# Performance work log

Measured on AMD Instinct MI355X. Metric: run time of the kernel, lower is better.

Reference implementation:

```python
import jax, jax.numpy as jnp
import numpy as np

B, N, M, D_MODEL, D_K, D_V = 8, 2048, 2048, 1024, 1024, 1024
NEG = -1000000000.0


def setup_inputs() -> dict:
    key = jax.random.key(0)
    ks = jax.random.split(key, 10)
    s = 1.0 / np.sqrt(D_MODEL)
    return {
        "querys": jax.random.normal(ks[0], (B, N, D_MODEL), jnp.float32),
        "keys": jax.random.normal(ks[1], (B, M, D_MODEL), jnp.float32),
        "values": jax.random.normal(ks[2], (B, M, D_MODEL), jnp.float32),
        "mask": jax.random.randint(ks[3], (N, M), 0, 2, jnp.int32),
        "Wq": jax.random.normal(ks[4], (D_K, D_MODEL), jnp.float32) * s,
        "bq": jnp.zeros((D_K,), jnp.float32),
        "Wk": jax.random.normal(ks[5], (D_K, D_MODEL), jnp.float32) * s,
        "bk": jnp.zeros((D_K,), jnp.float32),
        "Wv": jax.random.normal(ks[6], (D_V, D_MODEL), jnp.float32) * s,
        "bv": jnp.zeros((D_V,), jnp.float32),
    }


def reference(querys, keys, values, mask, Wq, bq, Wk, bk, Wv, bv):
    # Linear projections (torch Linear: x @ W.T + b)
    q = querys @ Wq.T + bq          # [B, N, Dk]
    k = keys @ Wk.T + bk            # [B, M, Dk]
    v = values @ Wv.T + bv          # [B, M, Dv]
    # Original computes QK^T via broadcast mul+sum; GEMM form is identical math.
    # NOTE: no 1/sqrt(d) scaling, matching the source.
    scores = jnp.einsum('bnd,bmd->bnm', q, k)  # [B, N, M]
    scores = jnp.where(mask[None, :, :] == 0, NEG, scores)
    weights = jax.nn.softmax(scores, axis=2)
    out = jnp.einsum('bnm,bmd->bnd', weights, v)  # [B, N, Dv]
    return out
```

## Files before the change

### kernel.cpp

```cpp
#include <hip/hip_runtime.h>
#include <cstdint>

typedef __bf16 bf16_t;
typedef __bf16 bf16x8 __attribute__((ext_vector_type(8)));
typedef float f32x4 __attribute__((ext_vector_type(4)));

#define AS1 __attribute__((address_space(1)))
#define AS3 __attribute__((address_space(3)))

__device__ __forceinline__ void gload_lds16(const bf16_t* g, bf16_t* l) {
    __builtin_amdgcn_global_load_lds((const AS1 void*)g, (AS3 void*)l, 16, 0, 0);
}
__device__ __forceinline__ f32x4 mfma_bf16(bf16x8 a, bf16x8 b, f32x4 c) {
    return __builtin_amdgcn_mfma_f32_16x16x32_bf16(a, b, c, 0, 0, 0);
}

template <bool SPLIT, int BIAS, int OUTMODE>
__global__ __launch_bounds__(512, 2) void gemm256(
    const bf16_t* __restrict__ Ah, const bf16_t* __restrict__ Al, long long strideA, int lda,
    const bf16_t* __restrict__ Bh, const bf16_t* __restrict__ Bl, long long strideB, int ldb,
    void* __restrict__ C0, void* __restrict__ C1, long long strideC, int ldc,
    const float* __restrict__ bias, int K)
{
    __shared__ bf16_t lds[4 * 16384];

    int bx = blockIdx.x, by = blockIdx.y, bz = blockIdx.z;
    {
        const int gx = gridDim.x, gy = gridDim.y, gz = gridDim.z;
        const int n = gx * gy * gz;
        if ((n & 7) == 0) {
            int lin = bx + gx * (by + gy * bz);
            lin = (lin & 7) * (n >> 3) + (lin >> 3);
            bx = lin % gx; lin /= gx;
            by = lin % gy; bz = lin / gy;
        }
    }

    const int rowBase = by * 256;
    const int colBase = bx * 256;
    const bf16_t* AhB = Ah + (long long)bz * strideA;
    const bf16_t* BhB = Bh + (long long)bz * strideB;
    const bf16_t* AlB = SPLIT ? Al + (long long)bz * strideA : nullptr;
    const bf16_t* BlB = SPLIT ? Bl + (long long)bz * strideB : nullptr;

    const int t = threadIdx.x;
    const int lane = t & 63;
    const int w = t >> 6;
    const int wm = w >> 2;
    const int wn = w & 3;

    const int r0 = t >> 2;
    const int sl8 = ((t & 3) ^ ((r0 >> 1) & 3)) * 8;
    const long long aoff0 = (long long)(rowBase + r0) * lda + sl8;
    const long long aoff1 = (long long)(rowBase + r0 + 128) * lda + sl8;
    const long long boff0 = (long long)(colBase + r0) * ldb + sl8;
    const long long boff1 = (long long)(colBase + r0 + 128) * ldb + sl8;

    const int NT = SPLIT ? (K >> 5) * 3 : (K >> 5);

    auto tsrc = [&](int jt, const bf16_t*& sA, const bf16_t*& sB, long long& k0) {
        if (SPLIT) {
            const int chunk = jt / 3;
            const int term = jt - chunk * 3;
            k0 = (long long)chunk * 32;
            sA = (term == 2) ? AlB : AhB;
            sB = (term == 1) ? BlB : BhB;
        } else {
            k0 = (long long)jt * 32;
            sA = AhB; sB = BhB;
        }
    };

    f32x4 acc[8][4] = {};

    for (int jt = 0; jt < 3; ++jt) {
        const bf16_t *sA, *sB; long long k0;
        tsrc(jt, sA, sB, k0);
        bf16_t* db = lds + jt * 16384;
        gload_lds16(sA + aoff0 + k0, db + t * 8);
        gload_lds16(sA + aoff1 + k0, db + 4096 + t * 8);
        gload_lds16(sB + boff0 + k0, db + 8192 + t * 8);
        gload_lds16(sB + boff1 + k0, db + 12288 + t * 8);
    }
    asm volatile("s_waitcnt vmcnt(8)" ::: "memory");
    __builtin_amdgcn_s_barrier();

    const int fr = lane & 15;
    const int kqs = ((lane >> 4) ^ ((lane >> 1) & 3)) * 8;

    for (int j = 0; j < NT; ++j) {
        const bf16_t* bufA = lds + (j & 3) * 16384;
        const bf16_t* bufB = bufA + 8192;

        const int jt = j + 3;
        if (jt < NT) {
            const bf16_t *sA, *sB; long long k0;
            tsrc(jt, sA, sB, k0);
            bf16_t* db = lds + (jt & 3) * 16384;
            gload_lds16(sA + aoff0 + k0, db + t * 8);
            gload_lds16(sA + aoff1 + k0, db + 4096 + t * 8);
            gload_lds16(sB + boff0 + k0, db + 8192 + t * 8);
            gload_lds16(sB + boff1 + k0, db + 12288 + t * 8);
        }

        bf16x8 a[8], b[4];
#pragma unroll
        for (int mi = 0; mi < 8; mi++)
            a[mi] = *(const bf16x8*)&bufA[(wm * 128 + mi * 16 + fr) * 32 + kqs];
#pragma unroll
        for (int ni = 0; ni < 4; ni++)
            b[ni] = *(const bf16x8*)&bufB[(wn * 64 + ni * 16 + fr) * 32 + kqs];

        __builtin_amdgcn_s_setprio(1);
#pragma unroll
        for (int mi = 0; mi < 8; mi++)
#pragma unroll
            for (int ni = 0; ni < 4; ni++)
                acc[mi][ni] = mfma_bf16(a[mi], b[ni], acc[mi][ni]);
        __builtin_amdgcn_s_setprio(0);

        if (j + 1 < NT) {
            if (j < NT - 3)       asm volatile("s_waitcnt vmcnt(8)" ::: "memory");
            else if (j == NT - 3) asm volatile("s_waitcnt vmcnt(4)" ::: "memory");
            else                  asm volatile("s_waitcnt vmcnt(0)" ::: "memory");
            __builtin_amdgcn_s_barrier();
        }
    }

    const int fc = lane & 15;
    const int fr4 = (lane >> 4) * 4;
#pragma unroll
    for (int mi = 0; mi < 8; mi++)
#pragma unroll
        for (int ni = 0; ni < 4; ni++)
#pragma unroll
            for (int rg = 0; rg < 4; rg++) {
                const int row = rowBase + wm * 128 + mi * 16 + fr4 + rg;
                const int col = colBase + wn * 64 + ni * 16 + fc;
                float v = acc[mi][ni][rg];
                if (BIAS == 1) v += bias[col];
                else if (BIAS == 2) v += bias[row];
                const long long off = (long long)bz * strideC + (long long)row * ldc + col;
                if (OUTMODE == 0) {
                    ((float*)C0)[off] = v;
                } else if (OUTMODE == 1) {
                    ((bf16_t*)C0)[off] = (bf16_t)v;
                } else {
                    const bf16_t h = (bf16_t)v;
                    ((bf16_t*)C0)[off] = h;
                    ((bf16_t*)C1)[off] = (bf16_t)(v - (float)h);
                }
            }
}

__global__ __launch_bounds__(256) void split_f32(const float* __restrict__ x,
                                                 bf16_t* __restrict__ h,
                                                 bf16_t* __restrict__ l)
{
    const long long i = ((long long)blockIdx.x * 256 + threadIdx.x) * 4;
    const float4 v = *(const float4*)&x[i];
    bf16_t hh[4], ll[4];
    const float vv[4] = {v.x, v.y, v.z, v.w};
#pragma unroll
    for (int j = 0; j < 4; j++) {
        hh[j] = (bf16_t)vv[j];
        ll[j] = (bf16_t)(vv[j] - (float)hh[j]);
    }
    *(short4*)&h[i] = *(short4*)hh;
    *(short4*)&l[i] = *(short4*)ll;
}

__global__ __launch_bounds__(256) void cast_f32(const float* __restrict__ x,
                                                bf16_t* __restrict__ y)
{
    const long long i = ((long long)blockIdx.x * 256 + threadIdx.x) * 4;
    const float4 v = *(const float4*)&x[i];
    bf16_t hh[4] = {(bf16_t)v.x, (bf16_t)v.y, (bf16_t)v.z, (bf16_t)v.w};
    *(short4*)&y[i] = *(short4*)hh;
}

__global__ __launch_bounds__(256) void softmax_rows(const float* __restrict__ S,
                                                    bf16_t* __restrict__ P,
                                                    const int* __restrict__ mask,
                                                    int n0)
{
    __shared__ float red[4];
    const long long r = blockIdx.x;
    const float* row = S + r * 2048;
    const int* mrow = mask + (long long)(n0 + (int)(r & 2047)) * 2048;
    const int t = threadIdx.x;

    float v[8];
#pragma unroll
    for (int i = 0; i < 8; i++) {
        const int j = i * 256 + t;
        v[i] = (mrow[j] != 0) ? row[j] : -1000000000.0f;
    }
    float m = v[0];
#pragma unroll
    for (int i = 1; i < 8; i++) m = fmaxf(m, v[i]);
#pragma unroll
    for (int off = 32; off; off >>= 1) m = fmaxf(m, __shfl_xor(m, off));
    if ((t & 63) == 0) red[t >> 6] = m;
    __syncthreads();
    const float rowmax = fmaxf(fmaxf(red[0], red[1]), fmaxf(red[2], red[3]));
    __syncthreads();

    float sum = 0.0f;
    float e[8];
#pragma unroll
    for (int i = 0; i < 8; i++) { e[i] = __expf(v[i] - rowmax); sum += e[i]; }
#pragma unroll
    for (int off = 32; off; off >>= 1) sum += __shfl_xor(sum, off);
    if ((t & 63) == 0) red[t >> 6] = sum;
    __syncthreads();
    const float inv = 1.0f / (red[0] + red[1] + red[2] + red[3]);

    bf16_t* prow = P + r * 2048;
#pragma unroll
    for (int i = 0; i < 8; i++) prow[i * 256 + t] = (bf16_t)(e[i] * inv);
}

extern "C" void kernel_launch(void* const* d_in, const int* in_sizes, int n_in,
                              void* d_out, int out_size, void* d_ws, size_t ws_size,
                              hipStream_t stream) {
    constexpr int Bb = 8, N = 2048, M = 2048, D = 1024;
    constexpr long long MB = 1LL << 20;

    const float* querys = (const float*)d_in[0];
    const float* keys   = (const float*)d_in[1];
    const float* values = (const float*)d_in[2];
    const int*   mask   = (const int*)d_in[3];
    const float* Wq = (const float*)d_in[4];
    const float* bq = (const float*)d_in[5];
    const float* Wk = (const float*)d_in[6];
    const float* bk = (const float*)d_in[7];
    const float* Wv = (const float*)d_in[8];
    const float* bv = (const float*)d_in[9];
    float* out = (float*)d_out;

    const long long w = (long long)ws_size;
    auto needB = [&](long long cb) { return 10 * MB + cb * 52 * MB; };
    int CB = 0;
    if      (w >= needB(8)) CB = 8;
    else if (w >= needB(4)) CB = 4;
    else if (w >= needB(2)) CB = 2;
    else if (w >= needB(1)) CB = 1;
    const bool batched = (CB != 0);
    int NCH = N;
    if (!batched) {
        CB = 1;
        NCH = (w >= 38 * MB + 512 * 2048 * 6) ? 512 : 256;
    }

    char* ws = (char*)d_ws;
    long long o = 0;
    auto carve = [&](long long bytes) { char* p = ws + o; o += bytes; return p; };
    bf16_t* WqH = (bf16_t*)carve(2 * MB);
    bf16_t* WqL = (bf16_t*)carve(2 * MB);
    bf16_t* WkH = (bf16_t*)carve(2 * MB);
    bf16_t* WkL = (bf16_t*)carve(2 * MB);
    bf16_t* WvB = (bf16_t*)carve(2 * MB);
    bf16_t* XH  = (bf16_t*)carve((long long)CB * 4 * MB);
    bf16_t* XL  = (bf16_t*)carve((long long)CB * 4 * MB);
    bf16_t* QH  = (bf16_t*)carve((long long)CB * 4 * MB);
    bf16_t* QL  = (bf16_t*)carve((long long)CB * 4 * MB);
    bf16_t* KH  = (bf16_t*)carve((long long)CB * 4 * MB);
    bf16_t* KL  = (bf16_t*)carve((long long)CB * 4 * MB);
    bf16_t* VT  = (bf16_t*)carve((long long)CB * 4 * MB);
    float*  S   = (float*)carve(batched ? (long long)CB * N * M * 4 : (long long)NCH * 2048 * 4);
    bf16_t* P   = (bf16_t*)carve(batched ? (long long)CB * N * M * 2 : (long long)NCH * 2048 * 2);

    dim3 blk(256), blkG(512);
    const long long grpElems = (long long)CB * N * D;

    split_f32<<<dim3((D * D) / 1024), blk, 0, stream>>>(Wq, WqH, WqL);
    split_f32<<<dim3((D * D) / 1024), blk, 0, stream>>>(Wk, WkH, WkL);
    cast_f32<<<dim3((D * D) / 1024), blk, 0, stream>>>(Wv, WvB);

    for (int b0 = 0; b0 < Bb; b0 += CB) {
        const long long xoff = (long long)b0 * N * D;
        split_f32<<<dim3(grpElems / 1024), blk, 0, stream>>>(querys + xoff, XH, XL);
        gemm256<true, 1, 2><<<dim3(D / 256, CB * N / 256, 1), blkG, 0, stream>>>(
            XH, XL, 0, D, WqH, WqL, 0, D, QH, QL, 0, D, bq, D);
        split_f32<<<dim3(grpElems / 1024), blk, 0, stream>>>(keys + xoff, XH, XL);
        gemm256<true, 1, 2><<<dim3(D / 256, CB * M / 256, 1), blkG, 0, stream>>>(
            XH, XL, 0, D, WkH, WkL, 0, D, KH, KL, 0, D, bk, D);
        cast_f32<<<dim3(grpElems / 1024), blk, 0, stream>>>(values + xoff, XH);
        gemm256<false, 2, 1><<<dim3(M / 256, D / 256, CB), blkG, 0, stream>>>(
            WvB, nullptr, 0, D, XH, nullptr, (long long)M * D, D,
            VT, nullptr, (long long)D * M, M, bv, D);

        if (batched) {
            gemm256<true, 0, 0><<<dim3(M / 256, N / 256, CB), blkG, 0, stream>>>(
                QH, QL, (long long)N * D, D,
                KH, KL, (long long)M * D, D,
                S, nullptr, (long long)N * M, M, nullptr, D);
            softmax_rows<<<dim3(CB * N), blk, 0, stream>>>(S, P, mask, 0);
            gemm256<false, 0, 0><<<dim3(D / 256, N / 256, CB), blkG, 0, stream>>>(
                P, nullptr, (long long)N * M, M,
                VT, nullptr, (long long)D * M, M,
                out + xoff, nullptr, (long long)N * D, D, nullptr, M);
        } else {
            for (int z = 0; z < CB; z++) {
                for (int n0 = 0; n0 < N; n0 += NCH) {
                    gemm256<true, 0, 0><<<dim3(M / 256, NCH / 256, 1), blkG, 0, stream>>>(
                        QH + ((long long)z * N + n0) * D, QL + ((long long)z * N + n0) * D, 0, D,
                        KH + (long long)z * M * D, KL + (long long)z * M * D, 0, D,
                        S, nullptr, 0, M, nullptr, D);
                    softmax_rows<<<dim3(NCH), blk, 0, stream>>>(S, P, mask, n0);
                    gemm256<false, 0, 0><<<dim3(D / 256, NCH / 256, 1), blkG, 0, stream>>>(
                        P, nullptr, 0, M, VT + (long long)z * D * M, nullptr, 0, M,
                        out + ((long long)(b0 + z) * N + n0) * D, nullptr, 0, D, nullptr, M);
                }
            }
        }
    }
    (void)in_sizes; (void)n_in; (void)out_size;
}
```

Before: 1.005 ms.

## Prefetch next tile's LDS fragments into registers during MFMA in GEMM

Restructures the GEMM main loop to double-buffer A fragments in registers: the next tile's A fragments are read from LDS before the current tile's MFMAs, and B fragments are read after them. The loop is unrolled by two to alternate register buffers, and the vmcnt waits are tightened so the next stage has landed before the barrier. The aim is to hide LDS read latency behind matrix-core work, at the cost of more registers and waiting earlier for global-to-LDS loads.

```diff
diff --git a/kernel.cpp b/kernel.cpp
--- a/kernel.cpp
+++ b/kernel.cpp
@@ -71,60 +71,66 @@
         }
     };
 
-    f32x4 acc[8][4] = {};
-
-    for (int jt = 0; jt < 3; ++jt) {
+    auto stage = [&](int jt) {
         const bf16_t *sA, *sB; long long k0;
         tsrc(jt, sA, sB, k0);
-        bf16_t* db = lds + jt * 16384;
+        bf16_t* db = lds + (jt & 3) * 16384;
         gload_lds16(sA + aoff0 + k0, db + t * 8);
         gload_lds16(sA + aoff1 + k0, db + 4096 + t * 8);
         gload_lds16(sB + boff0 + k0, db + 8192 + t * 8);
         gload_lds16(sB + boff1 + k0, db + 12288 + t * 8);
-    }
-    asm volatile("s_waitcnt vmcnt(8)" ::: "memory");
+    };
+
+    f32x4 acc[8][4] = {};
+
+    stage(0); stage(1); stage(2);
+    asm volatile("s_waitcnt vmcnt(4)" ::: "memory");
     __builtin_amdgcn_s_barrier();
 
     const int fr = lane & 15;
     const int kqs = ((lane >> 4) ^ ((lane >> 1) & 3)) * 8;
 
-    for (int j = 0; j < NT; ++j) {
-        const bf16_t* bufA = lds + (j & 3) * 16384;
-        const bf16_t* bufB = bufA + 8192;
-
-        const int jt = j + 3;
-        if (jt < NT) {
-            const bf16_t *sA, *sB; long long k0;
-            tsrc(jt, sA, sB, k0);
-            bf16_t* db = lds + (jt & 3) * 16384;
-            gload_lds16(sA + aoff0 + k0, db + t * 8);
-            gload_lds16(sA + aoff1 + k0, db + 4096 + t * 8);
-            gload_lds16(sB + boff0 + k0, db + 8192 + t * 8);
-            gload_lds16(sB + boff1 + k0, db + 12288 + t * 8);
-        }
-
-        bf16x8 a[8], b[4];
+    bf16x8 A0[8], A1[8], Bf[4];
+    {
+        const bf16_t* bufA = lds;
+        const bf16_t* bufB = lds + 8192;
 #pragma unroll
         for (int mi = 0; mi < 8; mi++)
-            a[mi] = *(const bf16x8*)&bufA[(wm * 128 + mi * 16 + fr) * 32 + kqs];
+            A0[mi] = *(const bf16x8*)&bufA[(wm * 128 + mi * 16 + fr) * 32 + kqs];
 #pragma unroll
         for (int ni = 0; ni < 4; ni++)
-            b[ni] = *(const bf16x8*)&bufB[(wn * 64 + ni * 16 + fr) * 32 + kqs];
-
+            Bf[ni] = *(const bf16x8*)&bufB[(wn * 64 + ni * 16 + fr) * 32 + kqs];
+    }
+
+    auto body = [&](int j, bf16x8 (&cur)[8], bf16x8 (&nxt)[8]) {
+        if (j + 3 < NT) stage(j + 3);
+        const bf16_t* nbufA = lds + ((j + 1) & 3) * 16384;
+        if (j + 1 < NT) {
+#pragma unroll
+            for (int mi = 0; mi < 8; mi++)
+                nxt[mi] = *(const bf16x8*)&nbufA[(wm * 128 + mi * 16 + fr) * 32 + kqs];
+        }
         __builtin_amdgcn_s_setprio(1);
 #pragma unroll
         for (int mi = 0; mi < 8; mi++)
 #pragma unroll
             for (int ni = 0; ni < 4; ni++)
-                acc[mi][ni] = mfma_bf16(a[mi], b[ni], acc[mi][ni]);
+                acc[mi][ni] = mfma_bf16(cur[mi], Bf[ni], acc[mi][ni]);
         __builtin_amdgcn_s_setprio(0);
-
         if (j + 1 < NT) {
-            if (j < NT - 3)       asm volatile("s_waitcnt vmcnt(8)" ::: "memory");
-            else if (j == NT - 3) asm volatile("s_waitcnt vmcnt(4)" ::: "memory");
-            else                  asm volatile("s_waitcnt vmcnt(0)" ::: "memory");
+            const bf16_t* nbufB = nbufA + 8192;
+#pragma unroll
+            for (int ni = 0; ni < 4; ni++)
+                Bf[ni] = *(const bf16x8*)&nbufB[(wn * 64 + ni * 16 + fr) * 32 + kqs];
+            if (j + 3 < NT) asm volatile("s_waitcnt vmcnt(4)" ::: "memory");
+            else            asm volatile("s_waitcnt vmcnt(0)" ::: "memory");
             __builtin_amdgcn_s_barrier();
         }
+    };
+
+    for (int j = 0; j < NT; j += 2) {
+        body(j, A0, A1);
+        if (j + 1 < NT) body(j + 1, A1, A0);
     }
 
     const int fc = lane & 15;
```

After: 1.010 ms. No clear change (+0.5%).

## Compute V projection as X·Wv^T with transposed vectorized epilogue, fuse weight prep

Applied to the files above, without the earlier changes.

The V projection is reoriented so it runs as a single flattened GEMM over all batch rows, like the Q and K projections. A new epilogue mode writes the transposed VT layout directly, using 4-wide bf16 vector stores along M. The three weight split/cast kernels are merged into one launch, and the s_setprio wrapping around the MFMA loop is removed. The transposed store is strided across columns, which may coalesce less well, and removing setprio could change wave scheduling.

```diff
diff --git a/kernel.cpp b/kernel.cpp
--- a/kernel.cpp
+++ b/kernel.cpp
@@ -20,7 +20,7 @@
     const bf16_t* __restrict__ Ah, const bf16_t* __restrict__ Al, long long strideA, int lda,
     const bf16_t* __restrict__ Bh, const bf16_t* __restrict__ Bl, long long strideB, int ldb,
     void* __restrict__ C0, void* __restrict__ C1, long long strideC, int ldc,
-    const float* __restrict__ bias, int K)
+    const float* __restrict__ bias, int K, int zrows)
 {
     __shared__ bf16_t lds[4 * 16384];
 
@@ -71,17 +71,19 @@
         }
     };
 
-    f32x4 acc[8][4] = {};
-
-    for (int jt = 0; jt < 3; ++jt) {
+    auto stage = [&](int jt) {
         const bf16_t *sA, *sB; long long k0;
         tsrc(jt, sA, sB, k0);
-        bf16_t* db = lds + jt * 16384;
+        bf16_t* db = lds + (jt & 3) * 16384;
         gload_lds16(sA + aoff0 + k0, db + t * 8);
         gload_lds16(sA + aoff1 + k0, db + 4096 + t * 8);
         gload_lds16(sB + boff0 + k0, db + 8192 + t * 8);
         gload_lds16(sB + boff1 + k0, db + 12288 + t * 8);
-    }
+    };
+
+    f32x4 acc[8][4] = {};
+
+    stage(0); stage(1); stage(2);
     asm volatile("s_waitcnt vmcnt(8)" ::: "memory");
     __builtin_amdgcn_s_barrier();
 
@@ -92,16 +94,7 @@
         const bf16_t* bufA = lds + (j & 3) * 16384;
         const bf16_t* bufB = bufA + 8192;
 
-        const int jt = j + 3;
-        if (jt < NT) {
-            const bf16_t *sA, *sB; long long k0;
-            tsrc(jt, sA, sB, k0);
-            bf16_t* db = lds + (jt & 3) * 16384;
-            gload_lds16(sA + aoff0 + k0, db + t * 8);
-            gload_lds16(sA + aoff1 + k0, db + 4096 + t * 8);
-            gload_lds16(sB + boff0 + k0, db + 8192 + t * 8);
-            gload_lds16(sB + boff1 + k0, db + 12288 + t * 8);
-        }
+        if (j + 3 < NT) stage(j + 3);
 
         bf16x8 a[8], b[4];
 #pragma unroll
@@ -111,13 +104,11 @@
         for (int ni = 0; ni < 4; ni++)
             b[ni] = *(const bf16x8*)&bufB[(wn * 64 + ni * 16 + fr) * 32 + kqs];
 
-        __builtin_amdgcn_s_setprio(1);
 #pragma unroll
         for (int mi = 0; mi < 8; mi++)
 #pragma unroll
             for (int ni = 0; ni < 4; ni++)
                 acc[mi][ni] = mfma_bf16(a[mi], b[ni], acc[mi][ni]);
-        __builtin_amdgcn_s_setprio(0);
 
         if (j + 1 < NT) {
             if (j < NT - 3)       asm volatile("s_waitcnt vmcnt(8)" ::: "memory");
@@ -129,6 +120,29 @@
 
     const int fc = lane & 15;
     const int fr4 = (lane >> 4) * 4;
+
+    if (OUTMODE == 3) {
+        const int zb = rowBase / zrows;
+        const int mBase = rowBase - zb * zrows;
+#pragma unroll
+        for (int mi = 0; mi < 8; mi++)
+#pragma unroll
+            for (int ni = 0; ni < 4; ni++) {
+                const int m0 = mBase + wm * 128 + mi * 16 + fr4;
+                const int col = colBase + wn * 64 + ni * 16 + fc;
+                bf16_t q[4];
+#pragma unroll
+                for (int rg = 0; rg < 4; rg++) {
+                    float v = acc[mi][ni][rg];
+                    if (BIAS == 1) v += bias[col];
+                    q[rg] = (bf16_t)v;
+                }
+                const long long off = (long long)zb * strideC + (long long)col * ldc + m0;
+                *(ushort4*)&((bf16_t*)C0)[off] = *(const ushort4*)q;
+            }
+        return;
+    }
+
 #pragma unroll
     for (int mi = 0; mi < 8; mi++)
 #pragma unroll
@@ -179,6 +193,27 @@
     *(short4*)&y[i] = *(short4*)hh;
 }
 
+__global__ __launch_bounds__(256) void prep_weights(
+    const float* __restrict__ Wq, const float* __restrict__ Wk, const float* __restrict__ Wv,
+    bf16_t* __restrict__ WqH, bf16_t* __restrict__ WqL,
+    bf16_t* __restrict__ WkH, bf16_t* __restrict__ WkL, bf16_t* __restrict__ WvB)
+{
+    const long long i = ((long long)blockIdx.x * 256 + threadIdx.x) * 4;
+    const int sel = blockIdx.y;
+    const float* x = (sel == 0) ? Wq : (sel == 1) ? Wk : Wv;
+    const float4 v = *(const float4*)&x[i];
+    const float vv[4] = {v.x, v.y, v.z, v.w};
+    bf16_t hh[4], ll[4];
+#pragma unroll
+    for (int j = 0; j < 4; j++) {
+        hh[j] = (bf16_t)vv[j];
+        ll[j] = (bf16_t)(vv[j] - (float)hh[j]);
+    }
+    if (sel == 0) { *(short4*)&WqH[i] = *(short4*)hh; *(short4*)&WqL[i] = *(short4*)ll; }
+    else if (sel == 1) { *(short4*)&WkH[i] = *(short4*)hh; *(short4*)&WkL[i] = *(short4*)ll; }
+    else { *(short4*)&WvB[i] = *(short4*)hh; }
+}
+
 __global__ __launch_bounds__(256) void softmax_rows(const float* __restrict__ S,
                                                     bf16_t* __restrict__ P,
                                                     const int* __restrict__ mask,
@@ -274,44 +309,43 @@
     dim3 blk(256), blkG(512);
     const long long grpElems = (long long)CB * N * D;
 
-    split_f32<<<dim3((D * D) / 1024), blk, 0, stream>>>(Wq, WqH, WqL);
-    split_f32<<<dim3((D * D) / 1024), blk, 0, stream>>>(Wk, WkH, WkL);
-    cast_f32<<<dim3((D * D) / 1024), blk, 0, stream>>>(Wv, WvB);
+    prep_weights<<<dim3((D * D) / 1024, 3), blk, 0, stream>>>(
+        Wq, Wk, Wv, WqH, WqL, WkH, WkL, WvB);
 
     for (int b0 = 0; b0 < Bb; b0 += CB) {
         const long long xoff = (long long)b0 * N * D;
         split_f32<<<dim3(grpElems / 1024), blk, 0, stream>>>(querys + xoff, XH, XL);
         gemm256<true, 1, 2><<<dim3(D / 256, CB * N / 256, 1), blkG, 0, stream>>>(
-            XH, XL, 0, D, WqH, WqL, 0, D, QH, QL, 0, D, bq, D);
+            XH, XL, 0, D, WqH, WqL, 0, D, QH, QL, 0, D, bq, D, 1);
         split_f32<<<dim3(grpElems / 1024), blk, 0, stream>>>(keys + xoff, XH, XL);
         gemm256<true, 1, 2><<<dim3(D / 256, CB * M / 256, 1), blkG, 0, stream>>>(
-            XH, XL, 0, D, WkH, WkL, 0, D, KH, KL, 0, D, bk, D);
+            XH, XL, 0, D, WkH, WkL, 0, D, KH, KL, 0, D, bk, D, 1);
         cast_f32<<<dim3(grpElems / 1024), blk, 0, stream>>>(values + xoff, XH);
-        gemm256<false, 2, 1><<<dim3(M / 256, D / 256, CB), blkG, 0, stream>>>(
-            WvB, nullptr, 0, D, XH, nullptr, (long long)M * D, D,
-            VT, nullptr, (long long)D * M, M, bv, D);
+        gemm256<false, 1, 3><<<dim3(D / 256, CB * M / 256, 1), blkG, 0, stream>>>(
+            XH, nullptr, 0, D, WvB, nullptr, 0, D,
+            VT, nullptr, (long long)D * M, M, bv, D, M);
 
         if (batched) {
             gemm256<true, 0, 0><<<dim3(M / 256, N / 256, CB), blkG, 0, stream>>>(
                 QH, QL, (long long)N * D, D,
                 KH, KL, (long long)M * D, D,
-                S, nullptr, (long long)N * M, M, nullptr, D);
+                S, nullptr, (long long)N * M, M, nullptr, D, 1);
             softmax_rows<<<dim3(CB * N), blk, 0, stream>>>(S, P, mask, 0);
             gemm256<false, 0, 0><<<dim3(D / 256, N / 256, CB), blkG, 0, stream>>>(
                 P, nullptr, (long long)N * M, M,
                 VT, nullptr, (long long)D * M, M,
-                out + xoff, nullptr, (long long)N * D, D, nullptr, M);
+                out + xoff, nullptr, (long long)N * D, D, nullptr, M, 1);
         } else {
             for (int z = 0; z < CB; z++) {
                 for (int n0 = 0; n0 < N; n0 += NCH) {
                     gemm256<true, 0, 0><<<dim3(M / 256, NCH / 256, 1), blkG, 0, stream>>>(
                         QH + ((long long)z * N + n0) * D, QL + ((long long)z * N + n0) * D, 0, D,
                         KH + (long long)z * M * D, KL + (long long)z * M * D, 0, D,
-                        S, nullptr, 0, M, nullptr, D);
+                        S, nullptr, 0, M, nullptr, D, 1);
                     softmax_rows<<<dim3(NCH), blk, 0, stream>>>(S, P, mask, n0);
                     gemm256<false, 0, 0><<<dim3(D / 256, NCH / 256, 1), blkG, 0, stream>>>(
                         P, nullptr, 0, M, VT + (long long)z * D * M, nullptr, 0, M,
-                        out + ((long long)(b0 + z) * N + n0) * D, nullptr, 0, D, nullptr, M);
+                        out + ((long long)(b0 + z) * N + n0) * D, nullptr, 0, D, nullptr, M, 1);
                 }
             }
         }
```

New measurement: 1.014 ms. No clear change (+0.9%).
